# Performance work log

Measured on AMD Instinct MI355X. Metric: run time of the kernel, lower is better.

Reference implementation:

```python
import jax, jax.numpy as jnp
import numpy as np
from jax import lax

WEIGHT_REG = 1e-06
BIAS_REG = 1e-06
DROP_REG = 1e-05
EPS = 1e-07
TEMP = 0.1


def setup_inputs() -> dict:
    key = jax.random.key(0)
    ks = jax.random.split(key, 9)
    B, T, D, H = 256, 512, 128, 128
    x = jax.random.normal(ks[0], (B, T, D), dtype=jnp.float32)
    # 0.05 scale keeps LSTM gates out of deep saturation
    weight_ih = jax.random.normal(ks[1], (4 * H, D), dtype=jnp.float32) * 0.05
    weight_hh = jax.random.normal(ks[2], (4 * H, H), dtype=jnp.float32) * 0.05
    bias_ih = jax.random.normal(ks[3], (4 * H,), dtype=jnp.float32) * 0.05
    bias_hh = jax.random.normal(ks[4], (4 * H,), dtype=jnp.float32) * 0.05
    p_logit = jax.random.normal(ks[5], (1,), dtype=jnp.float32)
    p_logit_rec = jax.random.normal(ks[6], (1,), dtype=jnp.float32)
    unif_x = jax.random.uniform(ks[7], (B, D), dtype=jnp.float32)
    unif_h = jax.random.uniform(ks[8], (B, H), dtype=jnp.float32)
    return {"x": x, "weight_ih": weight_ih, "weight_hh": weight_hh,
            "bias_ih": bias_ih, "bias_hh": bias_hh,
            "p_logit": p_logit, "p_logit_rec": p_logit_rec,
            "unif_x": unif_x, "unif_h": unif_h}


def _concrete_mask(u, p):
    # random_tensor = 1 - sigmoid((logit(p) + logit(u)) / temp)
    logit = (jnp.log(p + EPS) - jnp.log(1.0 - p + EPS)
             + jnp.log(u + EPS) - jnp.log(1.0 - u + EPS))
    return 1.0 - jax.nn.sigmoid(logit / TEMP)


def reference(x, weight_ih, weight_hh, bias_ih, bias_hh,
              p_logit, p_logit_rec, unif_x, unif_h):
    B, T, D = x.shape
    H = weight_hh.shape[1]
    p = jax.nn.sigmoid(p_logit)        # [1]
    p_rec = jax.nn.sigmoid(p_logit_rec)  # [1]

    # masks are sampled once (at t=0) and reused every timestep
    mask_x = _concrete_mask(unif_x, p)      # [B, D]
    mask_h = _concrete_mask(unif_h, p_rec)  # [B, H]

    x_d = x * mask_x[:, None, :] / (1.0 - p)  # dropout on input, all steps

    h0 = jnp.zeros((B, H), dtype=x.dtype)
    c0 = jnp.zeros((B, H), dtype=x.dtype)

    def step(carry, xt):
        h, c = carry
        hd = h * mask_h / (1.0 - p_rec)  # recurrent concrete dropout
        gates = xt @ weight_ih.T + bias_ih + hd @ weight_hh.T + bias_hh
        i_g, f_g, g_g, o_g = jnp.split(gates, 4, axis=-1)  # torch LSTMCell order
        c_new = jax.nn.sigmoid(f_g) * c + jax.nn.sigmoid(i_g) * jnp.tanh(g_g)
        h_new = jax.nn.sigmoid(o_g) * jnp.tanh(c_new)
        return (h_new, c_new), h_new

    (h_last, _), hs = lax.scan(step, (h0, c0), jnp.swapaxes(x_d, 0, 1))
    x_out = jnp.swapaxes(hs, 0, 1)  # [B, T, H]

    sum_kernel = jnp.sum(weight_ih ** 2)
    sum_rec = jnp.sum(weight_hh ** 2)
    sum_bias = jnp.sum(bias_ih ** 2) + jnp.sum(bias_hh ** 2)
    weights_reg = WEIGHT_REG * (sum_kernel / (1.0 - p) + sum_rec / (1.0 - p_rec))
    bias_reg = BIAS_REG * sum_bias
    ent_k = p * jnp.log(p) + (1.0 - p) * jnp.log(1.0 - p)
    ent_r = p_rec * jnp.log(p_rec) + (1.0 - p_rec) * jnp.log(1.0 - p_rec)
    drop_reg = DROP_REG * (D * ent_k + H * ent_r)
    regularization = weights_reg + bias_reg + drop_reg  # [1]

    return (x_out, h_last, regularization, p, p_rec)
```

## Files before the change

### kernel.cpp

```cpp
#include <hip/hip_runtime.h>
#include <cstddef>

#define NB 256
#define NT 512
#define ND 128
#define NH 128
#define NG 512
#define NM (NB * NT)
#define NMP (NM + 64)

constexpr float F_EPS  = 1e-7f;
constexpr float F_TEMP = 0.1f;

typedef _Float16 h2_t __attribute__((ext_vector_type(2)));
typedef _Float16 h4_t __attribute__((ext_vector_type(4)));
typedef _Float16 h8_t __attribute__((ext_vector_type(8)));
typedef float    fx4  __attribute__((ext_vector_type(4)));

#if defined(__has_builtin)
#  if __has_builtin(__builtin_amdgcn_fdot2)
#    define FDOT2(a, b, c) __builtin_amdgcn_fdot2((a), (b), (c), false)
#  endif
#endif
#ifndef FDOT2
#  define FDOT2(a, b, c) ((c) + (float)(a)[0] * (float)(b)[0] + (float)(a)[1] * (float)(b)[1])
#endif

__device__ __forceinline__ float fexp2(float x) {
#if defined(__has_builtin)
#  if __has_builtin(__builtin_amdgcn_exp2f)
    return __builtin_amdgcn_exp2f(x);
#  else
    return exp2f(x);
#  endif
#else
    return exp2f(x);
#endif
}
__device__ __forceinline__ float frcp(float x) {
#if defined(__has_builtin)
#  if __has_builtin(__builtin_amdgcn_rcpf)
    return __builtin_amdgcn_rcpf(x);
#  else
    return 1.0f / x;
#  endif
#else
    return 1.0f / x;
#endif
}
__device__ __forceinline__ float fsig(float x) {
    return frcp(1.0f + fexp2(x * -1.44269504088896f));
}
__device__ __forceinline__ float ftanh(float x) {
    return 1.0f - 2.0f * frcp(1.0f + fexp2(x * 2.885390081777927f));
}
__device__ __forceinline__ float sig(float x) { return 1.0f / (1.0f + expf(-x)); }

__device__ __forceinline__ void bar_lds() {
    asm volatile("s_waitcnt lgkmcnt(0)" ::: "memory");
    __builtin_amdgcn_sched_barrier(0);
    __builtin_amdgcn_s_barrier();
}

__global__ __launch_bounds__(256) void k_convert(const float* __restrict__ wih,
        const float* __restrict__ whh, _Float16* __restrict__ wih_h,
        _Float16* __restrict__ whh_h, float* __restrict__ partial) {
    int i = blockIdx.x * 256 + threadIdx.x;
    float4 a = ((const float4*)wih)[i];
    float4 b = ((const float4*)whh)[i];
    h4_t ah, bh;
    ah[0] = (_Float16)a.x; ah[1] = (_Float16)a.y; ah[2] = (_Float16)a.z; ah[3] = (_Float16)a.w;
    bh[0] = (_Float16)b.x; bh[1] = (_Float16)b.y; bh[2] = (_Float16)b.z; bh[3] = (_Float16)b.w;
    *(h4_t*)(wih_h + 4 * (size_t)i) = ah;
    *(h4_t*)(whh_h + 4 * (size_t)i) = bh;
    float sk = a.x * a.x + a.y * a.y + a.z * a.z + a.w * a.w;
    float sr = b.x * b.x + b.y * b.y + b.z * b.z + b.w * b.w;
    for (int off = 32; off; off >>= 1) {
        sk += __shfl_down(sk, off);
        sr += __shfl_down(sr, off);
    }
    if ((threadIdx.x & 63) == 0) {
        atomicAdd(partial + 0, sk);
        atomicAdd(partial + 1, sr);
    }
}

__global__ void k_tail(const float* __restrict__ bih, const float* __restrict__ bhh,
                       const float* __restrict__ pl, const float* __restrict__ plr,
                       const float* __restrict__ partial, float* __restrict__ out_tail) {
    __shared__ float red[8];
    int t = threadIdx.x;
    float v = bih[t], w2 = bhh[t];
    float sb = v * v + w2 * w2;
    for (int off = 32; off; off >>= 1) sb += __shfl_down(sb, off);
    int wid = t >> 6, lane = t & 63;
    if (lane == 0) red[wid] = sb;
    __syncthreads();
    if (t == 0) {
        float SB = 0.f;
        for (int i = 0; i < 8; i++) SB += red[i];
        float SK = partial[0], SR = partial[1];
        float p  = sig(pl[0]);
        float pr = sig(plr[0]);
        float wr = 1e-6f * (SK / (1.f - p) + SR / (1.f - pr));
        float br = 1e-6f * SB;
        float ek = p * logf(p) + (1.f - p) * logf(1.f - p);
        float er = pr * logf(pr) + (1.f - pr) * logf(1.f - pr);
        float dr = 1e-5f * ((float)ND * ek + (float)NH * er);
        out_tail[0] = wr + br + dr;
        out_tail[1] = p;
        out_tail[2] = pr;
    }
}

__global__ __launch_bounds__(256, 2) void k_gemm(const float* __restrict__ x,
        const _Float16* __restrict__ wih_h, const float* __restrict__ bih,
        const float* __restrict__ bhh, const float* __restrict__ pl,
        const float* __restrict__ unif_x, _Float16* __restrict__ Gp) {
    __shared__ _Float16 Alds[128 * 128];
    __shared__ _Float16 Wlds[128 * 128];
    __shared__ float sx[128];
    __shared__ float bsum[128];
    int t  = threadIdx.x;
    int m0 = blockIdx.x * 128;
    int j0 = blockIdx.y * 128;
    int b  = m0 >> 9;

    float p = sig(pl[0]);
    if (t < 128) {
        float u  = unif_x[b * ND + t];
        float lg = logf(p + F_EPS) - logf(1.f - p + F_EPS)
                 + logf(u + F_EPS) - logf(1.f - u + F_EPS);
        float mk = 1.f - sig(lg / F_TEMP);
        sx[t] = mk / (1.f - p);
    } else {
        int j = t - 128;
        bsum[j] = bih[j0 + j] + bhh[j0 + j];
    }
    __syncthreads();

#pragma unroll
    for (int i = 0; i < 8; i++) {
        int s   = i * 256 + t;
        int row = s >> 4;
        int s16 = s & 15;
        const float4* xp = (const float4*)(x + (size_t)(m0 + row) * ND + s16 * 8);
        float4 v0 = xp[0], v1 = xp[1];
        float4 s0 = *(const float4*)(sx + s16 * 8);
        float4 s1 = *(const float4*)(sx + s16 * 8 + 4);
        h8_t hv;
        hv[0] = (_Float16)(v0.x * s0.x); hv[1] = (_Float16)(v0.y * s0.y);
        hv[2] = (_Float16)(v0.z * s0.z); hv[3] = (_Float16)(v0.w * s0.w);
        hv[4] = (_Float16)(v1.x * s1.x); hv[5] = (_Float16)(v1.y * s1.y);
        hv[6] = (_Float16)(v1.z * s1.z); hv[7] = (_Float16)(v1.w * s1.w);
        *(h8_t*)(&Alds[(size_t)row * 128 + ((s16 ^ (row & 7)) << 3)]) = hv;
        h8_t wv = *(const h8_t*)(wih_h + (size_t)(j0 + row) * ND + s16 * 8);
        *(h8_t*)(&Wlds[(size_t)row * 128 + ((s16 ^ (row & 7)) << 3)]) = wv;
    }
    __syncthreads();

    int w  = t >> 6, l = t & 63;
    int lr = l & 15, lg = l >> 4;
    fx4 acc[2][8] = {};
#pragma unroll
    for (int kk = 0; kk < 4; kk++) {
        h8_t af[2], bf[8];
#pragma unroll
        for (int mt = 0; mt < 2; mt++) {
            int r = 32 * w + 16 * mt + lr;
            af[mt] = *(const h8_t*)(&Alds[(size_t)r * 128 + (((4 * kk + lg) ^ (r & 7)) << 3)]);
        }
#pragma unroll
        for (int nt = 0; nt < 8; nt++) {
            int r = 16 * nt + lr;
            bf[nt] = *(const h8_t*)(&Wlds[(size_t)r * 128 + (((4 * kk + lg) ^ (r & 7)) << 3)]);
        }
#pragma unroll
        for (int mt = 0; mt < 2; mt++)
#pragma unroll
            for (int nt = 0; nt < 8; nt++)
                acc[mt][nt] = __builtin_amdgcn_mfma_f32_16x16x32_f16(af[mt], bf[nt], acc[mt][nt], 0, 0, 0);
    }

#pragma unroll
    for (int mt = 0; mt < 2; mt++)
#pragma unroll
        for (int nt = 0; nt < 8; nt++) {
            int j = j0 + 16 * nt + lr;
            int m = m0 + 32 * w + 16 * mt + 4 * lg;
            float bv = bsum[16 * nt + lr];
            h4_t o;
#pragma unroll
            for (int q = 0; q < 4; q++) o[q] = (_Float16)(acc[mt][nt][q] + bv);
            *(h4_t*)(Gp + (size_t)j * NMP + m) = o;
        }
}

__global__ __launch_bounds__(256, 1) void k_lstm(const _Float16* __restrict__ Gp,
        const _Float16* __restrict__ whh_h, const float* __restrict__ plr,
        const float* __restrict__ unif_h,
        float* __restrict__ xout, float* __restrict__ hlast) {
    __shared__ _Float16 hd[2][128];
    int b    = blockIdx.x;
    int tid  = threadIdx.x;
    int l    = tid & 63;
    int wv   = tid >> 6;
    int n    = wv * 32 + (l & 31);
    int half = l >> 5;

    h2_t w[4][32];
#pragma unroll
    for (int gq = 0; gq < 4; gq++) {
        const _Float16* wr = whh_h + (size_t)(gq * 128 + n) * NH + 64 * half;
#pragma unroll
        for (int i = 0; i < 8; i++) {
            h8_t a = *(const h8_t*)(wr + 8 * i);
#pragma unroll
            for (int q = 0; q < 4; q++)
                w[gq][4 * i + q] = (h2_t){a[2 * q], a[2 * q + 1]};
        }
    }

    float pr = sig(plr[0]);
    float msk;
    {
        float u  = unif_h[b * NH + n];
        float lg = logf(pr + F_EPS) - logf(1.f - pr + F_EPS)
                 + logf(u + F_EPS) - logf(1.f - u + F_EPS);
        float mk = 1.f - sig(lg / F_TEMP);
        msk = mk / (1.f - pr);
    }
    float h = 0.f, c = 0.f;
    if (half == 0) hd[0][n] = (_Float16)0.f;

    const _Float16* gp0 = Gp + (size_t)(0 * 128 + n) * NMP + (size_t)b * NT;
    const _Float16* gp1 = Gp + (size_t)(1 * 128 + n) * NMP + (size_t)b * NT;
    const _Float16* gp2 = Gp + (size_t)(2 * 128 + n) * NMP + (size_t)b * NT;
    const _Float16* gp3 = Gp + (size_t)(3 * 128 + n) * NMP + (size_t)b * NT;
    float* xo = xout + (size_t)b * NT * NH + n;

    h8_t g0 = *(const h8_t*)(gp0);
    h8_t g1 = *(const h8_t*)(gp1);
    h8_t g2 = *(const h8_t*)(gp2);
    h8_t g3 = *(const h8_t*)(gp3);
    __syncthreads();

    for (int w8 = 0; w8 < NT / 8; w8++) {
#pragma unroll
        for (int gq = 0; gq < 4; gq++)
#pragma unroll
            for (int i = 0; i < 32; i++) asm volatile("" : "+v"(w[gq][i]));
        h8_t n0 = g0, n1 = g1, n2 = g2, n3 = g3;
        if (w8 + 1 < NT / 8) {
            n0 = *(const h8_t*)(gp0 + 8 * (w8 + 1));
            n1 = *(const h8_t*)(gp1 + 8 * (w8 + 1));
            n2 = *(const h8_t*)(gp2 + 8 * (w8 + 1));
            n3 = *(const h8_t*)(gp3 + 8 * (w8 + 1));
        }
#pragma unroll
        for (int e = 0; e < 8; e++) {
            const _Float16* hb = &hd[e & 1][64 * half];
            float a0a = 0.f, a0b = 0.f, a1a = 0.f, a1b = 0.f;
            float a2a = 0.f, a2b = 0.f, a3a = 0.f, a3b = 0.f;
#pragma unroll
            for (int i = 0; i < 8; i++) {
                h8_t hv = *(const h8_t*)(hb + 8 * i);
                h2_t h0 = (h2_t){hv[0], hv[1]}, h1v = (h2_t){hv[2], hv[3]};
                h2_t h2v = (h2_t){hv[4], hv[5]}, h3v = (h2_t){hv[6], hv[7]};
                a0a = FDOT2(h0, w[0][4 * i + 0], a0a);
                a0b = FDOT2(h1v, w[0][4 * i + 1], a0b);
                a0a = FDOT2(h2v, w[0][4 * i + 2], a0a);
                a0b = FDOT2(h3v, w[0][4 * i + 3], a0b);
                a1a = FDOT2(h0, w[1][4 * i + 0], a1a);
                a1b = FDOT2(h1v, w[1][4 * i + 1], a1b);
                a1a = FDOT2(h2v, w[1][4 * i + 2], a1a);
                a1b = FDOT2(h3v, w[1][4 * i + 3], a1b);
                a2a = FDOT2(h0, w[2][4 * i + 0], a2a);
                a2b = FDOT2(h1v, w[2][4 * i + 1], a2b);
                a2a = FDOT2(h2v, w[2][4 * i + 2], a2a);
                a2b = FDOT2(h3v, w[2][4 * i + 3], a2b);
                a3a = FDOT2(h0, w[3][4 * i + 0], a3a);
                a3b = FDOT2(h1v, w[3][4 * i + 1], a3b);
                a3a = FDOT2(h2v, w[3][4 * i + 2], a3a);
                a3b = FDOT2(h3v, w[3][4 * i + 3], a3b);
            }
            float s0 = a0a + a0b, s1 = a1a + a1b;
            float s2 = a2a + a2b, s3 = a3a + a3b;
            s0 += __shfl_xor(s0, 32, 64);
            s1 += __shfl_xor(s1, 32, 64);
            s2 += __shfl_xor(s2, 32, 64);
            s3 += __shfl_xor(s3, 32, 64);
            s0 += (float)g0[e];
            s1 += (float)g1[e];
            s2 += (float)g2[e];
            s3 += (float)g3[e];
            float iv = fsig(s0), fv = fsig(s1);
            float gv = ftanh(s2), ov = fsig(s3);
            c = fv * c + iv * gv;
            h = ov * ftanh(c);
            if (half == 0) {
                hd[(e & 1) ^ 1][n] = (_Float16)(h * msk);
                xo[(size_t)(8 * w8 + e) * NH] = h;
            }
            bar_lds();
        }
        g0 = n0; g1 = n1; g2 = n2; g3 = n3;
    }
    if (half == 0) hlast[(size_t)b * NH + n] = h;
}

extern "C" void kernel_launch(void* const* d_in, const int* in_sizes, int n_in,
                              void* d_out, int out_size, void* d_ws, size_t ws_size,
                              hipStream_t stream) {
    const float* x   = (const float*)d_in[0];
    const float* wih = (const float*)d_in[1];
    const float* whh = (const float*)d_in[2];
    const float* bih = (const float*)d_in[3];
    const float* bhh = (const float*)d_in[4];
    const float* pl  = (const float*)d_in[5];
    const float* plr = (const float*)d_in[6];
    const float* ux  = (const float*)d_in[7];
    const float* uh  = (const float*)d_in[8];

    float* out   = (float*)d_out;
    float* xout  = out;
    float* hlast = out + (size_t)NB * NT * NH;
    float* tail  = hlast + (size_t)NB * NH;

    _Float16* G     = (_Float16*)d_ws;
    _Float16* wih_h = (_Float16*)((char*)d_ws + (size_t)NG * NMP * 2);
    _Float16* whh_h = wih_h + (size_t)NG * ND;
    float*    partial = (float*)(whh_h + (size_t)NG * NH);

    hipMemsetAsync(partial, 0, 2 * sizeof(float), stream);

    k_convert<<<64, 256, 0, stream>>>(wih, whh, wih_h, whh_h, partial);

    dim3 gg(NM / 128, NG / 128);
    k_gemm<<<gg, 256, 0, stream>>>(x, wih_h, bih, bhh, pl, ux, G);

    k_tail<<<1, 512, 0, stream>>>(bih, bhh, pl, plr, partial, tail);

    k_lstm<<<NB, 256, 0, stream>>>(G, whh_h, plr, uh, xout, hlast);
}
```

Baseline: 377.3 us.

## Split LSTM recurrent dot products across four lane groups with 512-thread blocks

The recurrent kernel now uses 512 threads per batch row. Each hidden unit's 128-long dot product is split over four 16-lane groups instead of two 32-lane halves, then reduced with two xor shuffles. Per-thread weight registers and serial FDOT2 work per timestep are halved, which shortens the critical path of each sequential step. The cost is an extra shuffle stage, more waves contending at every per-step barrier, and gate prefetch shrunk to 4 timesteps.

```diff
diff --git a/kernel.cpp b/kernel.cpp
--- a/kernel.cpp
+++ b/kernel.cpp
@@ -196,28 +196,29 @@
         }
 }
 
-__global__ __launch_bounds__(256, 1) void k_lstm(const _Float16* __restrict__ Gp,
+__global__ __launch_bounds__(512) __attribute__((amdgpu_waves_per_eu(2, 2)))
+void k_lstm(const _Float16* __restrict__ Gp,
         const _Float16* __restrict__ whh_h, const float* __restrict__ plr,
         const float* __restrict__ unif_h,
         float* __restrict__ xout, float* __restrict__ hlast) {
     __shared__ _Float16 hd[2][128];
-    int b    = blockIdx.x;
-    int tid  = threadIdx.x;
-    int l    = tid & 63;
-    int wv   = tid >> 6;
-    int n    = wv * 32 + (l & 31);
-    int half = l >> 5;
-
-    h2_t w[4][32];
+    int b   = blockIdx.x;
+    int tid = threadIdx.x;
+    int l   = tid & 63;
+    int wv  = tid >> 6;
+    int n   = wv * 16 + (l & 15);
+    int q   = l >> 4;
+
+    h2_t w[4][16];
 #pragma unroll
     for (int gq = 0; gq < 4; gq++) {
-        const _Float16* wr = whh_h + (size_t)(gq * 128 + n) * NH + 64 * half;
-#pragma unroll
-        for (int i = 0; i < 8; i++) {
+        const _Float16* wr = whh_h + (size_t)(gq * 128 + n) * NH + 32 * q;
+#pragma unroll
+        for (int i = 0; i < 4; i++) {
             h8_t a = *(const h8_t*)(wr + 8 * i);
 #pragma unroll
-            for (int q = 0; q < 4; q++)
-                w[gq][4 * i + q] = (h2_t){a[2 * q], a[2 * q + 1]};
+            for (int pq = 0; pq < 4; pq++)
+                w[gq][4 * i + pq] = (h2_t){a[2 * pq], a[2 * pq + 1]};
         }
     }
 
@@ -231,7 +232,7 @@
         msk = mk / (1.f - pr);
     }
     float h = 0.f, c = 0.f;
-    if (half == 0) hd[0][n] = (_Float16)0.f;
+    if (q == 0) hd[0][n] = (_Float16)0.f;
 
     const _Float16* gp0 = Gp + (size_t)(0 * 128 + n) * NMP + (size_t)b * NT;
     const _Float16* gp1 = Gp + (size_t)(1 * 128 + n) * NMP + (size_t)b * NT;
@@ -239,53 +240,59 @@
     const _Float16* gp3 = Gp + (size_t)(3 * 128 + n) * NMP + (size_t)b * NT;
     float* xo = xout + (size_t)b * NT * NH + n;
 
-    h8_t g0 = *(const h8_t*)(gp0);
-    h8_t g1 = *(const h8_t*)(gp1);
-    h8_t g2 = *(const h8_t*)(gp2);
-    h8_t g3 = *(const h8_t*)(gp3);
+    h4_t g0 = *(const h4_t*)(gp0);
+    h4_t g1 = *(const h4_t*)(gp1);
+    h4_t g2 = *(const h4_t*)(gp2);
+    h4_t g3 = *(const h4_t*)(gp3);
     __syncthreads();
 
-    for (int w8 = 0; w8 < NT / 8; w8++) {
+    for (int w4 = 0; w4 < NT / 4; w4++) {
 #pragma unroll
         for (int gq = 0; gq < 4; gq++)
 #pragma unroll
-            for (int i = 0; i < 32; i++) asm volatile("" : "+v"(w[gq][i]));
-        h8_t n0 = g0, n1 = g1, n2 = g2, n3 = g3;
-        if (w8 + 1 < NT / 8) {
-            n0 = *(const h8_t*)(gp0 + 8 * (w8 + 1));
-            n1 = *(const h8_t*)(gp1 + 8 * (w8 + 1));
-            n2 = *(const h8_t*)(gp2 + 8 * (w8 + 1));
-            n3 = *(const h8_t*)(gp3 + 8 * (w8 + 1));
-        }
-#pragma unroll
-        for (int e = 0; e < 8; e++) {
-            const _Float16* hb = &hd[e & 1][64 * half];
-            float a0a = 0.f, a0b = 0.f, a1a = 0.f, a1b = 0.f;
-            float a2a = 0.f, a2b = 0.f, a3a = 0.f, a3b = 0.f;
-#pragma unroll
-            for (int i = 0; i < 8; i++) {
-                h8_t hv = *(const h8_t*)(hb + 8 * i);
-                h2_t h0 = (h2_t){hv[0], hv[1]}, h1v = (h2_t){hv[2], hv[3]};
-                h2_t h2v = (h2_t){hv[4], hv[5]}, h3v = (h2_t){hv[6], hv[7]};
-                a0a = FDOT2(h0, w[0][4 * i + 0], a0a);
-                a0b = FDOT2(h1v, w[0][4 * i + 1], a0b);
-                a0a = FDOT2(h2v, w[0][4 * i + 2], a0a);
-                a0b = FDOT2(h3v, w[0][4 * i + 3], a0b);
-                a1a = FDOT2(h0, w[1][4 * i + 0], a1a);
-                a1b = FDOT2(h1v, w[1][4 * i + 1], a1b);
-                a1a = FDOT2(h2v, w[1][4 * i + 2], a1a);
-                a1b = FDOT2(h3v, w[1][4 * i + 3], a1b);
-                a2a = FDOT2(h0, w[2][4 * i + 0], a2a);
-                a2b = FDOT2(h1v, w[2][4 * i + 1], a2b);
-                a2a = FDOT2(h2v, w[2][4 * i + 2], a2a);
-                a2b = FDOT2(h3v, w[2][4 * i + 3], a2b);
-                a3a = FDOT2(h0, w[3][4 * i + 0], a3a);
-                a3b = FDOT2(h1v, w[3][4 * i + 1], a3b);
-                a3a = FDOT2(h2v, w[3][4 * i + 2], a3a);
-                a3b = FDOT2(h3v, w[3][4 * i + 3], a3b);
+            for (int i = 0; i < 16; i++) asm volatile("" : "+v"(w[gq][i]));
+        h4_t n0 = g0, n1 = g1, n2 = g2, n3 = g3;
+        if (w4 + 1 < NT / 4) {
+            n0 = *(const h4_t*)(gp0 + 4 * (w4 + 1));
+            n1 = *(const h4_t*)(gp1 + 4 * (w4 + 1));
+            n2 = *(const h4_t*)(gp2 + 4 * (w4 + 1));
+            n3 = *(const h4_t*)(gp3 + 4 * (w4 + 1));
+        }
+#pragma unroll
+        for (int e = 0; e < 4; e++) {
+            const _Float16* hb = &hd[e & 1][32 * q];
+            h8_t hv[4];
+#pragma unroll
+            for (int r = 0; r < 4; r++) hv[r] = *(const h8_t*)(hb + 8 * r);
+            float sa0 = 0.f, sb0 = 0.f, sa1 = 0.f, sb1 = 0.f;
+            float sa2 = 0.f, sb2 = 0.f, sa3 = 0.f, sb3 = 0.f;
+#pragma unroll
+            for (int r = 0; r < 4; r++) {
+                h2_t x0 = (h2_t){hv[r][0], hv[r][1]}, x1 = (h2_t){hv[r][2], hv[r][3]};
+                h2_t x2 = (h2_t){hv[r][4], hv[r][5]}, x3 = (h2_t){hv[r][6], hv[r][7]};
+                sa0 = FDOT2(x0, w[0][4 * r + 0], sa0);
+                sb0 = FDOT2(x1, w[0][4 * r + 1], sb0);
+                sa0 = FDOT2(x2, w[0][4 * r + 2], sa0);
+                sb0 = FDOT2(x3, w[0][4 * r + 3], sb0);
+                sa1 = FDOT2(x0, w[1][4 * r + 0], sa1);
+                sb1 = FDOT2(x1, w[1][4 * r + 1], sb1);
+                sa1 = FDOT2(x2, w[1][4 * r + 2], sa1);
+                sb1 = FDOT2(x3, w[1][4 * r + 3], sb1);
+                sa2 = FDOT2(x0, w[2][4 * r + 0], sa2);
+                sb2 = FDOT2(x1, w[2][4 * r + 1], sb2);
+                sa2 = FDOT2(x2, w[2][4 * r + 2], sa2);
+                sb2 = FDOT2(x3, w[2][4 * r + 3], sb2);
+                sa3 = FDOT2(x0, w[3][4 * r + 0], sa3);
+                sb3 = FDOT2(x1, w[3][4 * r + 1], sb3);
+                sa3 = FDOT2(x2, w[3][4 * r + 2], sa3);
+                sb3 = FDOT2(x3, w[3][4 * r + 3], sb3);
             }
-            float s0 = a0a + a0b, s1 = a1a + a1b;
-            float s2 = a2a + a2b, s3 = a3a + a3b;
+            float s0 = sa0 + sb0, s1 = sa1 + sb1;
+            float s2 = sa2 + sb2, s3 = sa3 + sb3;
+            s0 += __shfl_xor(s0, 16, 64);
+            s1 += __shfl_xor(s1, 16, 64);
+            s2 += __shfl_xor(s2, 16, 64);
+            s3 += __shfl_xor(s3, 16, 64);
             s0 += __shfl_xor(s0, 32, 64);
             s1 += __shfl_xor(s1, 32, 64);
             s2 += __shfl_xor(s2, 32, 64);
@@ -298,15 +305,15 @@
             float gv = ftanh(s2), ov = fsig(s3);
             c = fv * c + iv * gv;
             h = ov * ftanh(c);
-            if (half == 0) {
+            if (q == 0) {
                 hd[(e & 1) ^ 1][n] = (_Float16)(h * msk);
-                xo[(size_t)(8 * w8 + e) * NH] = h;
+                xo[(size_t)(4 * w4 + e) * NH] = h;
             }
             bar_lds();
         }
         g0 = n0; g1 = n1; g2 = n2; g3 = n3;
     }
-    if (half == 0) hlast[(size_t)b * NH + n] = h;
+    if (q == 0) hlast[(size_t)b * NH + n] = h;
 }
 
 extern "C" void kernel_launch(void* const* d_in, const int* in_sizes, int n_in,
@@ -341,5 +348,5 @@
 
     k_tail<<<1, 512, 0, stream>>>(bih, bhh, pl, plr, partial, tail);
 
-    k_lstm<<<NB, 256, 0, stream>>>(G, whh_h, plr, uh, xout, hlast);
-}
+    k_lstm<<<NB, 512, 0, stream>>>(G, whh_h, plr, uh, xout, hlast);
+}
```

Result: slower. 466.6 us (+23.7%).

## Pack two batch sequences per LSTM block and precompute dropout masks once

Applied to the files above, without the earlier changes.

The recurrent LSTM kernel now runs two batch rows per 512-thread block (128 blocks instead of 256) with separate LDS h buffers, so two independent recurrences share a CU and can hide each other's latency. The shared barrier now synchronises both sequences. The concrete-dropout masks for x and h are computed once in k_convert and stored as fp16, so the GEMM and LSTM kernels no longer recompute per-block logs and sigmoids. The trade-off is that half as many CUs run the serial recurrence, and the masks lose some precision from fp16 storage.

```diff
diff --git a/kernel.cpp b/kernel.cpp
--- a/kernel.cpp
+++ b/kernel.cpp
@@ -63,8 +63,11 @@
 }
 
 __global__ __launch_bounds__(256) void k_convert(const float* __restrict__ wih,
-        const float* __restrict__ whh, _Float16* __restrict__ wih_h,
-        _Float16* __restrict__ whh_h, float* __restrict__ partial) {
+        const float* __restrict__ whh, const float* __restrict__ pl,
+        const float* __restrict__ plr, const float* __restrict__ unif_x,
+        const float* __restrict__ unif_h, _Float16* __restrict__ wih_h,
+        _Float16* __restrict__ whh_h, _Float16* __restrict__ mask_x,
+        _Float16* __restrict__ mask_h, float* __restrict__ partial) {
     int i = blockIdx.x * 256 + threadIdx.x;
     float4 a = ((const float4*)wih)[i];
     float4 b = ((const float4*)whh)[i];
@@ -83,6 +86,26 @@
         atomicAdd(partial + 0, sk);
         atomicAdd(partial + 1, sr);
     }
+    float p;
+    const float* up;
+    _Float16* mp;
+    int mi;
+    if (i < 8192) { p = sig(pl[0]);  up = unif_x; mp = mask_x; mi = i; }
+    else          { p = sig(plr[0]); up = unif_h; mp = mask_h; mi = i - 8192; }
+    float4 u = ((const float4*)up)[mi];
+    float base = logf(p + F_EPS) - logf(1.f - p + F_EPS);
+    float inv  = 1.f / (1.f - p);
+    h4_t m4;
+    {
+        float uu[4] = {u.x, u.y, u.z, u.w};
+#pragma unroll
+        for (int e = 0; e < 4; ++e) {
+            float lg = base + logf(uu[e] + F_EPS) - logf(1.f - uu[e] + F_EPS);
+            float mk = 1.f - sig(lg / F_TEMP);
+            m4[e] = (_Float16)(mk * inv);
+        }
+    }
+    *(h4_t*)(mp + 4 * (size_t)mi) = m4;
 }
 
 __global__ void k_tail(const float* __restrict__ bih, const float* __restrict__ bhh,
@@ -115,28 +138,17 @@
 
 __global__ __launch_bounds__(256, 2) void k_gemm(const float* __restrict__ x,
         const _Float16* __restrict__ wih_h, const float* __restrict__ bih,
-        const float* __restrict__ bhh, const float* __restrict__ pl,
-        const float* __restrict__ unif_x, _Float16* __restrict__ Gp) {
+        const float* __restrict__ bhh, const _Float16* __restrict__ mask_x,
+        _Float16* __restrict__ Gp) {
     __shared__ _Float16 Alds[128 * 128];
     __shared__ _Float16 Wlds[128 * 128];
-    __shared__ float sx[128];
     __shared__ float bsum[128];
     int t  = threadIdx.x;
     int m0 = blockIdx.x * 128;
     int j0 = blockIdx.y * 128;
     int b  = m0 >> 9;
 
-    float p = sig(pl[0]);
-    if (t < 128) {
-        float u  = unif_x[b * ND + t];
-        float lg = logf(p + F_EPS) - logf(1.f - p + F_EPS)
-                 + logf(u + F_EPS) - logf(1.f - u + F_EPS);
-        float mk = 1.f - sig(lg / F_TEMP);
-        sx[t] = mk / (1.f - p);
-    } else {
-        int j = t - 128;
-        bsum[j] = bih[j0 + j] + bhh[j0 + j];
-    }
+    if (t < 128) bsum[t] = bih[j0 + t] + bhh[j0 + t];
     __syncthreads();
 
 #pragma unroll
@@ -146,13 +158,12 @@
         int s16 = s & 15;
         const float4* xp = (const float4*)(x + (size_t)(m0 + row) * ND + s16 * 8);
         float4 v0 = xp[0], v1 = xp[1];
-        float4 s0 = *(const float4*)(sx + s16 * 8);
-        float4 s1 = *(const float4*)(sx + s16 * 8 + 4);
+        h8_t mk = *(const h8_t*)(mask_x + (size_t)b * ND + s16 * 8);
         h8_t hv;
-        hv[0] = (_Float16)(v0.x * s0.x); hv[1] = (_Float16)(v0.y * s0.y);
-        hv[2] = (_Float16)(v0.z * s0.z); hv[3] = (_Float16)(v0.w * s0.w);
-        hv[4] = (_Float16)(v1.x * s1.x); hv[5] = (_Float16)(v1.y * s1.y);
-        hv[6] = (_Float16)(v1.z * s1.z); hv[7] = (_Float16)(v1.w * s1.w);
+        hv[0] = (_Float16)(v0.x * (float)mk[0]); hv[1] = (_Float16)(v0.y * (float)mk[1]);
+        hv[2] = (_Float16)(v0.z * (float)mk[2]); hv[3] = (_Float16)(v0.w * (float)mk[3]);
+        hv[4] = (_Float16)(v1.x * (float)mk[4]); hv[5] = (_Float16)(v1.y * (float)mk[5]);
+        hv[6] = (_Float16)(v1.z * (float)mk[6]); hv[7] = (_Float16)(v1.w * (float)mk[7]);
         *(h8_t*)(&Alds[(size_t)row * 128 + ((s16 ^ (row & 7)) << 3)]) = hv;
         h8_t wv = *(const h8_t*)(wih_h + (size_t)(j0 + row) * ND + s16 * 8);
         *(h8_t*)(&Wlds[(size_t)row * 128 + ((s16 ^ (row & 7)) << 3)]) = wv;
@@ -196,17 +207,18 @@
         }
 }
 
-__global__ __launch_bounds__(256, 1) void k_lstm(const _Float16* __restrict__ Gp,
-        const _Float16* __restrict__ whh_h, const float* __restrict__ plr,
-        const float* __restrict__ unif_h,
-        float* __restrict__ xout, float* __restrict__ hlast) {
-    __shared__ _Float16 hd[2][128];
-    int b    = blockIdx.x;
+__global__ __launch_bounds__(512) __attribute__((amdgpu_waves_per_eu(2, 2)))
+void k_lstm(const _Float16* __restrict__ Gp, const _Float16* __restrict__ whh_h,
+            const _Float16* __restrict__ maskh,
+            float* __restrict__ xout, float* __restrict__ hlast) {
+    __shared__ _Float16 hd[2][2][128];
     int tid  = threadIdx.x;
+    int sub  = tid >> 8;
     int l    = tid & 63;
-    int wv   = tid >> 6;
+    int wv   = (tid >> 6) & 3;
     int n    = wv * 32 + (l & 31);
     int half = l >> 5;
+    int b    = blockIdx.x * 2 + sub;
 
     h2_t w[4][32];
 #pragma unroll
@@ -221,17 +233,9 @@
         }
     }
 
-    float pr = sig(plr[0]);
-    float msk;
-    {
-        float u  = unif_h[b * NH + n];
-        float lg = logf(pr + F_EPS) - logf(1.f - pr + F_EPS)
-                 + logf(u + F_EPS) - logf(1.f - u + F_EPS);
-        float mk = 1.f - sig(lg / F_TEMP);
-        msk = mk / (1.f - pr);
-    }
+    float msk = (float)maskh[(size_t)b * NH + n];
     float h = 0.f, c = 0.f;
-    if (half == 0) hd[0][n] = (_Float16)0.f;
+    if (half == 0) hd[sub][0][n] = (_Float16)0.f;
 
     const _Float16* gp0 = Gp + (size_t)(0 * 128 + n) * NMP + (size_t)b * NT;
     const _Float16* gp1 = Gp + (size_t)(1 * 128 + n) * NMP + (size_t)b * NT;
@@ -259,30 +263,30 @@
         }
 #pragma unroll
         for (int e = 0; e < 8; e++) {
-            const _Float16* hb = &hd[e & 1][64 * half];
+            const _Float16* hb = &hd[sub][e & 1][64 * half];
             float a0a = 0.f, a0b = 0.f, a1a = 0.f, a1b = 0.f;
             float a2a = 0.f, a2b = 0.f, a3a = 0.f, a3b = 0.f;
 #pragma unroll
             for (int i = 0; i < 8; i++) {
                 h8_t hv = *(const h8_t*)(hb + 8 * i);
-                h2_t h0 = (h2_t){hv[0], hv[1]}, h1v = (h2_t){hv[2], hv[3]};
-                h2_t h2v = (h2_t){hv[4], hv[5]}, h3v = (h2_t){hv[6], hv[7]};
-                a0a = FDOT2(h0, w[0][4 * i + 0], a0a);
-                a0b = FDOT2(h1v, w[0][4 * i + 1], a0b);
-                a0a = FDOT2(h2v, w[0][4 * i + 2], a0a);
-                a0b = FDOT2(h3v, w[0][4 * i + 3], a0b);
-                a1a = FDOT2(h0, w[1][4 * i + 0], a1a);
-                a1b = FDOT2(h1v, w[1][4 * i + 1], a1b);
-                a1a = FDOT2(h2v, w[1][4 * i + 2], a1a);
-                a1b = FDOT2(h3v, w[1][4 * i + 3], a1b);
-                a2a = FDOT2(h0, w[2][4 * i + 0], a2a);
-                a2b = FDOT2(h1v, w[2][4 * i + 1], a2b);
-                a2a = FDOT2(h2v, w[2][4 * i + 2], a2a);
-                a2b = FDOT2(h3v, w[2][4 * i + 3], a2b);
-                a3a = FDOT2(h0, w[3][4 * i + 0], a3a);
-                a3b = FDOT2(h1v, w[3][4 * i + 1], a3b);
-                a3a = FDOT2(h2v, w[3][4 * i + 2], a3a);
-                a3b = FDOT2(h3v, w[3][4 * i + 3], a3b);
+                h2_t x0 = (h2_t){hv[0], hv[1]}, x1 = (h2_t){hv[2], hv[3]};
+                h2_t x2 = (h2_t){hv[4], hv[5]}, x3 = (h2_t){hv[6], hv[7]};
+                a0a = FDOT2(x0, w[0][4 * i + 0], a0a);
+                a0b = FDOT2(x1, w[0][4 * i + 1], a0b);
+                a0a = FDOT2(x2, w[0][4 * i + 2], a0a);
+                a0b = FDOT2(x3, w[0][4 * i + 3], a0b);
+                a1a = FDOT2(x0, w[1][4 * i + 0], a1a);
+                a1b = FDOT2(x1, w[1][4 * i + 1], a1b);
+                a1a = FDOT2(x2, w[1][4 * i + 2], a1a);
+                a1b = FDOT2(x3, w[1][4 * i + 3], a1b);
+                a2a = FDOT2(x0, w[2][4 * i + 0], a2a);
+                a2b = FDOT2(x1, w[2][4 * i + 1], a2b);
+                a2a = FDOT2(x2, w[2][4 * i + 2], a2a);
+                a2b = FDOT2(x3, w[2][4 * i + 3], a2b);
+                a3a = FDOT2(x0, w[3][4 * i + 0], a3a);
+                a3b = FDOT2(x1, w[3][4 * i + 1], a3b);
+                a3a = FDOT2(x2, w[3][4 * i + 2], a3a);
+                a3b = FDOT2(x3, w[3][4 * i + 3], a3b);
             }
             float s0 = a0a + a0b, s1 = a1a + a1b;
             float s2 = a2a + a2b, s3 = a3a + a3b;
@@ -299,7 +303,7 @@
             c = fv * c + iv * gv;
             h = ov * ftanh(c);
             if (half == 0) {
-                hd[(e & 1) ^ 1][n] = (_Float16)(h * msk);
+                hd[sub][(e & 1) ^ 1][n] = (_Float16)(h * msk);
                 xo[(size_t)(8 * w8 + e) * NH] = h;
             }
             bar_lds();
@@ -327,19 +331,22 @@
     float* hlast = out + (size_t)NB * NT * NH;
     float* tail  = hlast + (size_t)NB * NH;
 
-    _Float16* G     = (_Float16*)d_ws;
-    _Float16* wih_h = (_Float16*)((char*)d_ws + (size_t)NG * NMP * 2);
-    _Float16* whh_h = wih_h + (size_t)NG * ND;
-    float*    partial = (float*)(whh_h + (size_t)NG * NH);
+    _Float16* G      = (_Float16*)d_ws;
+    _Float16* wih_h  = G + (size_t)NG * NMP;
+    _Float16* whh_h  = wih_h + (size_t)NG * ND;
+    _Float16* mask_x = whh_h + (size_t)NG * NH;
+    _Float16* mask_h = mask_x + (size_t)NB * ND;
+    float*    partial = (float*)(mask_h + (size_t)NB * NH);
 
     hipMemsetAsync(partial, 0, 2 * sizeof(float), stream);
 
-    k_convert<<<64, 256, 0, stream>>>(wih, whh, wih_h, whh_h, partial);
+    k_convert<<<64, 256, 0, stream>>>(wih, whh, pl, plr, ux, uh,
+                                      wih_h, whh_h, mask_x, mask_h, partial);
 
     dim3 gg(NM / 128, NG / 128);
-    k_gemm<<<gg, 256, 0, stream>>>(x, wih_h, bih, bhh, pl, ux, G);
+    k_gemm<<<gg, 256, 0, stream>>>(x, wih_h, bih, bhh, mask_x, G);
 
     k_tail<<<1, 512, 0, stream>>>(bih, bhh, pl, plr, partial, tail);
 
-    k_lstm<<<NB, 256, 0, stream>>>(G, whh_h, plr, uh, xout, hlast);
-}
+    k_lstm<<<NB / 2, 512, 0, stream>>>(G, whh_h, mask_h, xout, hlast);
+}
```

Measured after the change: 549.1 us. +45.5%, slower.
